# Performance work log

Hardware: AMD Instinct MI355X
Metric: run time of the kernel (lower is better)

The kernel has to match this reference:

```python
import jax, jax.numpy as jnp
import numpy as np

T, B = 4096, 32
EP_LEN = 256
K = T // EP_LEN          # episodes per trajectory
LM = EP_LEN              # max episode length
S_DIM, C_DIM, M_DIM, L_DIM = 128, 32, 32, 32
E_S, E_C, H, A = 128, 64, 256, 16


def setup_inputs() -> dict:
    key = jax.random.key(0)
    ks = jax.random.split(key, 16)
    f = lambda i, shape: jax.random.normal(ks[i], shape, jnp.float32)
    inp = {
        "state": f(0, (T, B, S_DIM)),
        "latent_mean": f(1, (T, B, L_DIM)) * 0.1,
        "latent_logvar": f(2, (T, B, L_DIM)) * 0.1,
        "latent_mean_t": f(3, (T, B, L_DIM)) * 0.1,
        "latent_logvar_t": f(4, (T, B, L_DIM)) * 0.1,
        "agent_character": f(5, (T, B, C_DIM)),
        "mental_state": f(6, (T, B, M_DIM)),
        "partner_actions": jax.random.randint(ks[7], (LM, B), 0, A, jnp.int32),
    }
    # episode boundaries: done at the last step of each EP_LEN-long episode
    t = jnp.arange(T)
    inp["dones"] = jnp.broadcast_to(((t + 1) % EP_LEN == 0).astype(jnp.float32)[:, None], (T, B))
    sc = lambda fan: 1.0 / np.sqrt(fan)
    inp["W_se"] = f(8, (S_DIM, E_S)) * sc(S_DIM); inp["b_se"] = jnp.zeros((E_S,), jnp.float32)
    inp["W_ce"] = f(9, (C_DIM, E_C)) * sc(C_DIM); inp["b_ce"] = jnp.zeros((E_C,), jnp.float32)
    inp["W_sa"] = f(10, (E_S + E_C, H)) * sc(E_S + E_C); inp["b_sa"] = jnp.zeros((H,), jnp.float32)
    inp["W_h"] = f(11, (E_C + M_DIM, H)) * sc(E_C + M_DIM); inp["b_h"] = jnp.zeros((H,), jnp.float32)
    inp["Wi"] = f(12, (H, 3 * H)) * sc(H); inp["bi"] = jnp.zeros((3 * H,), jnp.float32)
    inp["Wh"] = f(13, (H, 3 * H)) * sc(H); inp["bh"] = jnp.zeros((3 * H,), jnp.float32)
    inp["W_out"] = f(14, (H, A)) * sc(H); inp["b_out"] = jnp.zeros((A,), jnp.float32)
    return inp


def _gru(h, x, Wi, bi, Wh, bh):
    gi = x @ Wi + bi
    gh = h @ Wh + bh
    ir, iz, inn = jnp.split(gi, 3, axis=-1)
    hr, hz, hn = jnp.split(gh, 3, axis=-1)
    r = jax.nn.sigmoid(ir + hr)
    z = jax.nn.sigmoid(iz + hz)
    n = jnp.tanh(inn + r * hn)
    return (1.0 - z) * n + z * h


def _episode_layout(d):  # d: [T] float dones -> (episode_id, pos_in_episode)
    started = jnp.concatenate([jnp.zeros((1,), bool), d[:-1] > 0.5])
    ep = jnp.cumsum(started.astype(jnp.int32))
    t = jnp.arange(d.shape[0])
    start = jax.lax.cummax(jnp.where(started, t, 0))
    return ep, t - start


def _to_episodes(x, ep, pos):  # x: [T, F] -> [K, LM, F]  (transform_timestep_to_batch)
    return jnp.zeros((K, LM) + x.shape[1:], x.dtype).at[ep, pos].set(x, mode="drop")


def _shift_padding_to_front(out, mask):  # out: [K, LM, D], mask: [K, LM]
    cnt = mask.sum(-1).astype(jnp.int32)
    src = jnp.arange(LM)[None, :] - (LM - cnt)[:, None]
    idx = jnp.clip(src, 0, LM - 1)
    ok = (src >= 0).astype(out.dtype)
    shifted = jnp.take_along_axis(out, idx[:, :, None], axis=1) * ok[:, :, None]
    return shifted, jnp.take_along_axis(mask, idx, axis=1) * ok


def _forward(state, latent_mean, latent_logvar, latent_mean_t, latent_logvar_t,
             agent_character, mental_state, partner_actions, dones,
             W_se, b_se, W_ce, b_ce, W_sa, b_sa, W_h, b_h, Wi, bi, Wh, bh, W_out, b_out):
    # ---- KL between consecutive-timestep posteriors ----
    lm = jnp.concatenate((latent_mean, latent_mean_t), axis=-1)
    lv = jnp.concatenate((latent_logvar, latent_logvar_t), axis=-1)
    gauss_dim = lm.shape[-1]
    all_m = jnp.concatenate((jnp.zeros((1,) + lm.shape[1:], lm.dtype), lm), axis=0)
    all_lv = jnp.concatenate((jnp.zeros((1,) + lv.shape[1:], lv.dtype), lv), axis=0)
    mu, m = all_m[1:], all_m[:-1]
    logE, logS = all_lv[1:], all_lv[:-1]
    kl = 0.5 * (jnp.sum(logS, -1) - jnp.sum(logE, -1) - gauss_dim
                + jnp.sum(jnp.exp(logE - logS), -1)
                + jnp.sum((m - mu) * (m - mu) / jnp.exp(logS), -1))  # [T,B]
    kl_loss = kl.sum(0).sum(0).mean()

    # ---- embeddings ----
    se = jax.nn.relu(state @ W_se + b_se)                         # [T,B,E_S]
    ce = jax.nn.relu(agent_character @ W_ce + b_ce)               # [T,B,E_C]
    sa = jnp.concatenate((se, ce), -1) @ W_sa + b_sa              # [T,B,H]
    hid = jnp.concatenate((ce, mental_state), -1) @ W_h + b_h     # [T,B,H]

    # ---- split trajectories into episodes (gather/scatter) ----
    ep, pos = jax.vmap(_episode_layout, in_axes=1, out_axes=0)(dones)  # [B,T] each
    to_ep = jax.vmap(_to_episodes, in_axes=(1, 0, 0), out_axes=0)
    k_sa = to_ep(sa, ep, pos)                                     # [B,K,LM,H]
    k_hid = to_ep(hid, ep, pos)                                   # [B,K,LM,H]
    k_d = to_ep(dones[..., None], ep, pos)[..., 0]                # [B,K,LM]
    mask = jax.vmap(lambda e, p: jnp.zeros((K, LM), jnp.float32).at[e, p].set(1.0, mode="drop"))(ep, pos)

    # ---- sequential RNN scan per episode (vectorized over B*K) ----
    h0 = k_hid[:, :, 0, :]                                        # [B,K,H]
    xs = (jnp.moveaxis(k_sa, 2, 0), jnp.moveaxis(k_hid, 2, 0), jnp.moveaxis(k_d, 2, 0))

    def step(h, xt):
        sa_t, hid_t, d_t = xt
        h = jnp.where(d_t[..., None] > 0.5, hid_t, h)             # reset to per-step init on done
        h = _gru(h, sa_t, Wi, bi, Wh, bh)
        return h, h

    _, ys = jax.lax.scan(step, h0, xs)                            # [LM,B,K,H]
    ys = jnp.moveaxis(ys, 0, 2)                                   # [B,K,LM,H]

    logits = (ys @ W_out + b_out) * mask[..., None]               # [B,K,LM,A]
    shifted, _ = jax.vmap(_shift_padding_to_front)(logits, mask)
    out = jnp.moveaxis(shifted.sum(1), 0, 1)                      # [LM,B,A]

    logp = jnp.take_along_axis(jax.nn.log_softmax(out, -1), partner_actions[..., None], -1)[..., 0]
    return kl_loss, logp.sum(-1)                                  # scalar, [LM]


def reference(state, latent_mean, latent_logvar, latent_mean_t, latent_logvar_t,
              agent_character, mental_state, partner_actions, dones,
              W_se, b_se, W_ce, b_ce, W_sa, b_sa, W_h, b_h, Wi, bi, Wh, bh, W_out, b_out):
    return _forward(state, latent_mean, latent_logvar, latent_mean_t, latent_logvar_t,
                    agent_character, mental_state, partner_actions, dones,
                    W_se, b_se, W_ce, b_ce, W_sa, b_sa, W_h, b_h, Wi, bi, Wh, bh, W_out, b_out)
```

## Files before the change

### kernel.cpp

```cpp
#include <hip/hip_runtime.h>
#include <math.h>

typedef short bf16x8 __attribute__((ext_vector_type(8)));
typedef float f32x4 __attribute__((ext_vector_type(4)));
typedef unsigned short u16;
typedef unsigned int u32;

#define T_DIM 4096
#define B_DIM 32

static constexpr size_t OFF_SE     = 0;
static constexpr size_t OFF_CE     = 33554432;
static constexpr size_t OFF_SA     = 50331648;
static constexpr size_t OFF_HID    = 117440512;
static constexpr size_t OFF_WHT    = 117964800;
static constexpr size_t OFF_WIT    = 118358016;
static constexpr size_t OFF_OUTACC = 118751232;
static constexpr size_t OFF_KLP    = 119799808;

__device__ __forceinline__ u16 f2bf(float x) {
    u32 b = __float_as_uint(x);
    u32 lsb = (b >> 16) & 1u;
    b += 0x7fffu + lsb;
    return (u16)(b >> 16);
}
__device__ __forceinline__ float bf2f(u16 u) {
    return __uint_as_float(((u32)u) << 16);
}
__device__ __forceinline__ float fsig(float x) {
    x = fminf(fmaxf(x, -30.f), 30.f);
    float e = __expf(x);
    return __fdividef(e, e + 1.f);
}
__device__ __forceinline__ float ftanh(float x) {
    x = fminf(fmaxf(x, -15.f), 15.f);
    float e = __expf(2.f * x);
    return __fdividef(e - 1.f, e + 1.f);
}

__global__ __launch_bounds__(256) void prep_kernel(const float* __restrict__ Wh,
                                                   const float* __restrict__ Wi,
                                                   u16* __restrict__ WhT,
                                                   u16* __restrict__ WiT) {
    int idx = blockIdx.x * 256 + threadIdx.x;
    if (idx < 196608) {
        int n = idx >> 8, k = idx & 255;
        WhT[idx] = f2bf(Wh[k * 768 + n]);
    } else {
        int i = idx - 196608;
        int n = i >> 8, k = i & 255;
        WiT[i] = f2bf(Wi[k * 768 + n]);
    }
}

__global__ __launch_bounds__(256) void prep2_kernel(const float* __restrict__ Wse,
                                                    const float* __restrict__ Wce,
                                                    const float* __restrict__ Wsa,
                                                    const float* __restrict__ Wwh,
                                                    u16* __restrict__ WTse,
                                                    u16* __restrict__ WTce,
                                                    u16* __restrict__ WTsa,
                                                    u16* __restrict__ WTh) {
    int idx = blockIdx.x * 256 + threadIdx.x;
    if (idx < 16384) {
        int n = idx >> 7, k = idx & 127;
        WTse[n * 128 + k] = f2bf(Wse[k * 128 + n]);
    } else if (idx < 18432) {
        int i = idx - 16384;
        int n = i >> 5, k = i & 31;
        WTce[n * 32 + k] = f2bf(Wce[k * 64 + n]);
    } else if (idx < 67584) {
        int i = idx - 18432;
        int n = i / 192, k = i % 192;
        WTsa[n * 192 + k] = f2bf(Wsa[k * 256 + n]);
    } else {
        int i = idx - 67584;
        int n = i / 96, k = i % 96;
        WTh[n * 96 + k] = f2bf(Wwh[k * 256 + n]);
    }
}

#define KLTERM(MU, LE, M, LS)                   \
    do {                                        \
        float _ls = (LS), _le = (LE);           \
        sS += _ls; sE += _le;                   \
        float _es = expf(-_ls);                 \
        sX += expf(_le) * _es;                  \
        float _dm = (M) - (MU);                 \
        sQ += _dm * _dm * _es;                  \
    } while (0)

__global__ __launch_bounds__(256) void kl_kernel(const float* __restrict__ lm,
                                                 const float* __restrict__ lv,
                                                 const float* __restrict__ lmt,
                                                 const float* __restrict__ lvt,
                                                 float* __restrict__ klp) {
    __shared__ float red[256];
    int tid = threadIdx.x;
    int idx = blockIdx.x * 256 + tid;
    float sS = 0.f, sE = 0.f, sX = 0.f, sQ = 0.f;
    const int cur = idx * 32;
    const int prv = cur - B_DIM * 32;
    const bool hasprev = (idx >= B_DIM);
    for (int half = 0; half < 2; half++) {
        const float* pm = half ? lmt : lm;
        const float* pv = half ? lvt : lv;
        for (int ch = 0; ch < 8; ch++) {
            float4 mu = *(const float4*)&pm[cur + ch * 4];
            float4 le = *(const float4*)&pv[cur + ch * 4];
            float4 m = make_float4(0.f, 0.f, 0.f, 0.f);
            float4 ls = make_float4(0.f, 0.f, 0.f, 0.f);
            if (hasprev) {
                m = *(const float4*)&pm[prv + ch * 4];
                ls = *(const float4*)&pv[prv + ch * 4];
            }
            KLTERM(mu.x, le.x, m.x, ls.x);
            KLTERM(mu.y, le.y, m.y, ls.y);
            KLTERM(mu.z, le.z, m.z, ls.z);
            KLTERM(mu.w, le.w, m.w, ls.w);
        }
    }
    float kl = 0.5f * (sS - sE - 64.0f + sX + sQ);
    red[tid] = kl;
    __syncthreads();
    for (int s = 128; s > 0; s >>= 1) {
        if (tid < s) red[tid] += red[tid + s];
        __syncthreads();
    }
    if (tid == 0) klp[blockIdx.x] = red[0];
}

__global__ __launch_bounds__(256) void gemm_k(const float* __restrict__ A32a,
                                              const u16* __restrict__ A16a,
                                              const u16* __restrict__ A16b,
                                              const u16* __restrict__ WT,
                                              const float* __restrict__ bias,
                                              u16* __restrict__ out,
                                              int mode, int K, int N, int do_relu) {
    __shared__ __align__(16) u16 As[64 * 40];
    const int tid = threadIdx.x;
    const int rows0 = blockIdx.x * 64;
    const int cols0 = blockIdx.y * 64;
    const int w16 = tid >> 6;
    const int lane = tid & 63;
    const int quad = lane >> 4;
    const int l15 = lane & 15;
    f32x4 acc[4];
    for (int i = 0; i < 4; i++) acc[i] = (f32x4){0.f, 0.f, 0.f, 0.f};
    const int nsteps = K >> 5;
    const int arow = tid >> 2, aseg = (tid & 3) << 3;
    for (int ks = 0; ks < nsteps; ks++) {
        const int grow = rows0 + arow;
        const int k0 = ks * 32 + aseg;
        if (mode == 0) {
            float4 v0 = *(const float4*)&A32a[grow * 128 + k0];
            float4 v1 = *(const float4*)&A32a[grow * 128 + k0 + 4];
            u16* d = &As[arow * 40 + aseg];
            d[0] = f2bf(v0.x); d[1] = f2bf(v0.y); d[2] = f2bf(v0.z); d[3] = f2bf(v0.w);
            d[4] = f2bf(v1.x); d[5] = f2bf(v1.y); d[6] = f2bf(v1.z); d[7] = f2bf(v1.w);
        } else if (mode == 1) {
            float4 v0 = *(const float4*)&A32a[grow * 32 + k0];
            float4 v1 = *(const float4*)&A32a[grow * 32 + k0 + 4];
            u16* d = &As[arow * 40 + aseg];
            d[0] = f2bf(v0.x); d[1] = f2bf(v0.y); d[2] = f2bf(v0.z); d[3] = f2bf(v0.w);
            d[4] = f2bf(v1.x); d[5] = f2bf(v1.y); d[6] = f2bf(v1.z); d[7] = f2bf(v1.w);
        } else if (mode == 2) {
            bf16x8 v = (k0 < 128) ? *(const bf16x8*)&A16a[grow * 128 + k0]
                                  : *(const bf16x8*)&A16b[grow * 64 + (k0 - 128)];
            *(bf16x8*)&As[arow * 40 + aseg] = v;
        } else {
            const int k6 = grow >> 6, w = (grow >> 5) & 1, bb = grow & 31;
            const int trow = (k6 * 256 + w * 255) * B_DIM + bb;
            for (int j = 0; j < 8; j++) {
                const int k = k0 + j;
                float v = (k < 64) ? bf2f(A16a[trow * 64 + k]) : A32a[trow * 32 + (k - 64)];
                As[arow * 40 + aseg + j] = f2bf(v);
            }
        }
        __syncthreads();
        bf16x8 af = *(const bf16x8*)&As[(w16 * 16 + l15) * 40 + quad * 8];
        const int kb = ks * 32 + quad * 8;
#pragma unroll
        for (int nt = 0; nt < 4; nt++) {
            bf16x8 bfr = *(const bf16x8*)&WT[(size_t)(cols0 + nt * 16 + l15) * K + kb];
            acc[nt] = __builtin_amdgcn_mfma_f32_16x16x32_bf16(af, bfr, acc[nt], 0, 0, 0);
        }
        __syncthreads();
    }
    for (int nt = 0; nt < 4; nt++) {
        const int c = cols0 + nt * 16 + l15;
        const float bv = bias[c];
        for (int r = 0; r < 4; r++) {
            const int row = rows0 + w16 * 16 + quad * 4 + r;
            float v = acc[nt][r] + bv;
            if (do_relu) v = fmaxf(v, 0.f);
            out[row * N + c] = f2bf(v);
        }
    }
}

__global__ void __launch_bounds__(512)
__attribute__((amdgpu_waves_per_eu(2, 2)))
gru6_kernel(const u16* __restrict__ hid,
            const u16* __restrict__ sa,
            const u16* __restrict__ WhT,
            const u16* __restrict__ WiT,
            const float* __restrict__ Wout,
            const float* __restrict__ bi,
            const float* __restrict__ bh,
            u16* __restrict__ gic_all,
            float* __restrict__ outacc) {
    __shared__ __align__(16) u16 whL[8 * 16 * 264];
    __shared__ __align__(16) u16 stage[64 * 264];
    __shared__ __align__(16) u16 hB[16 * 264];
    __shared__ __align__(16) u16 WoL[16 * 264];
    __shared__ __align__(16) float logL[32 * 16];
    __shared__ float bfold[768];
    __shared__ float bhnL[256];
    const int blk = blockIdx.x;
    const int b = blk >> 1, half = blk & 1;
    const int tid = threadIdx.x;
    const int lane = tid & 63, wv = tid >> 6;
    const int quad = lane >> 4, l15 = lane & 15;
    const int c0 = (tid & 63) * 4;
    u16* gic = gic_all + (size_t)blk * (256 * 768);

    for (int i = tid; i < 4096; i += 512) {
        const int s = i >> 9, rr = (i >> 5) & 15, seg = (i & 31) * 8;
        const int g = s * 6 + 5;
        *(bf16x8*)&whL[(s * 16 + rr) * 264 + seg] = *(const bf16x8*)&WhT[(g * 16 + rr) * 256 + seg];
    }
    for (int i = tid; i < 4096; i += 512) {
        const int a = i >> 8, k = i & 255;
        WoL[a * 264 + k] = f2bf(Wout[k * 16 + a]);
    }
    for (int c = tid; c < 768; c += 512) bfold[c] = (c < 512) ? (bi[c] + bh[c]) : bi[c];
    if (tid < 256) bhnL[tid] = bh[512 + tid];
    float hreg[4];
    {
        ushort4 hv = *(const ushort4*)&hid[(size_t)((((half << 3) + wv) << 6) + b) * 256 + c0];
        hreg[0] = bf2f(hv.x); hreg[1] = bf2f(hv.y);
        hreg[2] = bf2f(hv.z); hreg[3] = bf2f(hv.w);
        *(ushort4*)&hB[wv * 264 + c0] = hv;
        ushort4 z = make_ushort4(0, 0, 0, 0);
        *(ushort4*)&hB[(8 + wv) * 264 + c0] = z;
    }
    __syncthreads();

    bf16x8 wreg[5][8];
    for (int ch = 0; ch < 8; ch++) {
        for (int as = 0; as < 4; as++) {
            __syncthreads();
#pragma unroll
            for (int j = 0; j < 4; j++) {
                const int lin = j * 512 + tid;
                const int row = lin >> 5, seg = (lin & 31) * 8;
                const int pcs = as * 8 + (row >> 3), sql = row & 7;
                const int t = ((half << 3) + sql) * 256 + ch * 32 + pcs;
                *(bf16x8*)&stage[row * 264 + seg] =
                    *(const bf16x8*)&sa[((size_t)(t * 32 + b)) * 256 + seg];
            }
            __syncthreads();
            bf16x8 afr[4][8];
#pragma unroll
            for (int mt = 0; mt < 4; mt++)
#pragma unroll
                for (int ks = 0; ks < 8; ks++)
                    afr[mt][ks] = *(const bf16x8*)&stage[(mt * 16 + l15) * 264 + ks * 32 + quad * 8];
            bf16x8 wc[8], wn[8];
            {
                const u16* p = &WiT[((wv * 6) * 16 + l15) * 256 + quad * 8];
#pragma unroll
                for (int ks = 0; ks < 8; ks++) wc[ks] = *(const bf16x8*)&p[ks * 32];
            }
            for (int j = 0; j < 6; j++) {
                if (j < 5) {
                    const u16* p = &WiT[((wv * 6 + j + 1) * 16 + l15) * 256 + quad * 8];
#pragma unroll
                    for (int ks = 0; ks < 8; ks++) wn[ks] = *(const bf16x8*)&p[ks * 32];
                }
                const float bf = bfold[(wv * 6 + j) * 16 + l15];
#pragma unroll
                for (int mt = 0; mt < 4; mt++) {
                    f32x4 acc = (f32x4){0.f, 0.f, 0.f, 0.f};
#pragma unroll
                    for (int ks = 0; ks < 8; ks++)
                        acc = __builtin_amdgcn_mfma_f32_16x16x32_bf16(afr[mt][ks], wc[ks], acc, 0, 0, 0);
                    const int rbase = as * 64 + mt * 16 + quad * 4;
#pragma unroll
                    for (int r = 0; r < 4; r++)
                        gic[(size_t)(rbase + r) * 768 + (wv * 6 + j) * 16 + l15] = f2bf(acc[r] + bf);
                }
#pragma unroll
                for (int ks = 0; ks < 8; ks++) wc[ks] = wn[ks];
            }
        }
#pragma unroll
        for (int j = 0; j < 5; j++) {
            const u16* p = &WhT[((wv * 6 + j) * 16 + l15) * 256 + quad * 8];
#pragma unroll
            for (int ks = 0; ks < 8; ks++) wreg[j][ks] = *(const bf16x8*)&p[ks * 32];
        }
        __syncthreads();
        ushort4 pregi0, pregi1, pregi2;
        {
            const u16* gp0 = &gic[(size_t)(0 * 8 + wv) * 768];
            pregi0 = *(const ushort4*)&gp0[c0];
            pregi1 = *(const ushort4*)&gp0[256 + c0];
            pregi2 = *(const ushort4*)&gp0[512 + c0];
        }
        for (int pc = 0; pc < 32; pc++) {
            const int POS = ch * 32 + pc;
            __syncthreads();
            ushort4 g_r = pregi0;
            ushort4 g_z = pregi1;
            ushort4 g_n = pregi2;
            if (pc < 31) {
                const u16* gp = &gic[(size_t)((pc + 1) * 8 + wv) * 768];
                pregi0 = *(const ushort4*)&gp[c0];
                pregi1 = *(const ushort4*)&gp[256 + c0];
                pregi2 = *(const ushort4*)&gp[512 + c0];
            }
            bf16x8 af[8];
            if (POS == 255) {
                const u16* hp = &hid[(size_t)((((half << 3) + (l15 & 7)) << 6) + 32 + b) * 256 + quad * 8];
#pragma unroll
                for (int ks = 0; ks < 8; ks++) af[ks] = *(const bf16x8*)&hp[ks * 32];
            } else {
#pragma unroll
                for (int ks = 0; ks < 8; ks++)
                    af[ks] = *(const bf16x8*)&hB[l15 * 264 + ks * 32 + quad * 8];
            }
            if (wv == 7) {
                f32x4 acc = (f32x4){0.f, 0.f, 0.f, 0.f};
                if (POS == 255) {
#pragma unroll
                    for (int ks = 0; ks < 8; ks++) {
                        bf16x8 al = *(const bf16x8*)&hB[l15 * 264 + ks * 32 + quad * 8];
                        bf16x8 wo = *(const bf16x8*)&WoL[l15 * 264 + ks * 32 + quad * 8];
                        acc = __builtin_amdgcn_mfma_f32_16x16x32_bf16(al, wo, acc, 0, 0, 0);
                    }
                } else {
#pragma unroll
                    for (int ks = 0; ks < 8; ks++) {
                        bf16x8 wo = *(const bf16x8*)&WoL[l15 * 264 + ks * 32 + quad * 8];
                        acc = __builtin_amdgcn_mfma_f32_16x16x32_bf16(af[ks], wo, acc, 0, 0, 0);
                    }
                }
                float s = acc[0] + acc[1] + acc[2] + acc[3];
                s += __shfl_down(s, 32);
                s += __shfl_down(s, 16);
                if (lane < 16)
                    logL[(((pc + 31) & 31) << 4) + lane] = s;
            }
#pragma unroll
            for (int j = 0; j < 5; j++) {
                f32x4 acc = (f32x4){0.f, 0.f, 0.f, 0.f};
#pragma unroll
                for (int ks = 0; ks < 8; ks++)
                    acc = __builtin_amdgcn_mfma_f32_16x16x32_bf16(af[ks], wreg[j][ks], acc, 0, 0, 0);
                const int t = wv * 6 + j;
#pragma unroll
                for (int r = 0; r < 4; r++)
                    stage[(quad * 4 + r) * 776 + t * 16 + l15] = f2bf(acc[r]);
            }
            {
                const u16* p = &whL[(wv * 16 + l15) * 264 + quad * 8];
                f32x4 acc = (f32x4){0.f, 0.f, 0.f, 0.f};
#pragma unroll
                for (int ks = 0; ks < 8; ks++)
                    acc = __builtin_amdgcn_mfma_f32_16x16x32_bf16(af[ks], *(const bf16x8*)&p[ks * 32], acc, 0, 0, 0);
                const int t = wv * 6 + 5;
#pragma unroll
                for (int r = 0; r < 4; r++)
                    stage[(quad * 4 + r) * 776 + t * 16 + l15] = f2bf(acc[r]);
            }
            __syncthreads();
            if (POS == 255) {
                ushort4 hv = *(const ushort4*)&hid[(size_t)((((half << 3) + wv) << 6) + 32 + b) * 256 + c0];
                hreg[0] = bf2f(hv.x); hreg[1] = bf2f(hv.y);
                hreg[2] = bf2f(hv.z); hreg[3] = bf2f(hv.w);
            }
            ushort4 h_r = *(const ushort4*)&stage[wv * 776 + c0];
            ushort4 h_z = *(const ushort4*)&stage[wv * 776 + 256 + c0];
            ushort4 h_n = *(const ushort4*)&stage[wv * 776 + 512 + c0];
            const u16* grp = (const u16*)&g_r; const u16* gzp = (const u16*)&g_z;
            const u16* gnp = (const u16*)&g_n;
            const u16* hrp = (const u16*)&h_r; const u16* hzp = (const u16*)&h_z;
            const u16* hnp = (const u16*)&h_n;
            ushort4 hp4;
            u16* ho = (u16*)&hp4;
#pragma unroll
            for (int j = 0; j < 4; j++) {
                const float rv = fsig(bf2f(grp[j]) + bf2f(hrp[j]));
                const float zv = fsig(bf2f(gzp[j]) + bf2f(hzp[j]));
                const float nv = ftanh(bf2f(gnp[j]) + rv * (bf2f(hnp[j]) + bhnL[c0 + j]));
                hreg[j] = (1.f - zv) * nv + zv * hreg[j];
                ho[j] = f2bf(hreg[j]);
            }
            *(ushort4*)&hB[wv * 264 + c0] = hp4;
        }
        if (wv == 7) {
            const int s = lane >> 1, aoff = (lane & 1) << 3;
            const int P = (s == 31) ? (ch * 32 - 1) : (ch * 32 + s);
            if (P >= 0) {
                const float4* lp = (const float4*)&logL[(s << 4) + aoff];
                float* gpo = outacc + (size_t)half * 131072 + ((size_t)P * B_DIM + b) * 16 + aoff;
                *(float4*)&gpo[0] = lp[0];
                *(float4*)&gpo[4] = lp[1];
            }
        }
    }
    __syncthreads();
    if (wv == 7) {
        f32x4 acc = (f32x4){0.f, 0.f, 0.f, 0.f};
#pragma unroll
        for (int ks = 0; ks < 8; ks++) {
            bf16x8 al = *(const bf16x8*)&hB[l15 * 264 + ks * 32 + quad * 8];
            bf16x8 wo = *(const bf16x8*)&WoL[l15 * 264 + ks * 32 + quad * 8];
            acc = __builtin_amdgcn_mfma_f32_16x16x32_bf16(al, wo, acc, 0, 0, 0);
        }
        float s = acc[0] + acc[1] + acc[2] + acc[3];
        s += __shfl_down(s, 32);
        s += __shfl_down(s, 16);
        if (lane < 16)
            outacc[(size_t)half * 131072 + ((size_t)255 * B_DIM + b) * 16 + lane] = s;
    }
}

__global__ __launch_bounds__(64) void final_kernel(const float* __restrict__ outacc,
                                                   const int* __restrict__ pa,
                                                   const float* __restrict__ klp,
                                                   const float* __restrict__ bout,
                                                   float* __restrict__ dout) {
    const int lane = threadIdx.x;
    if (blockIdx.x == 256) {
        float s = 0.f;
        for (int j = 0; j < 8; j++) s += klp[lane + 64 * j];
        for (int off = 32; off > 0; off >>= 1) s += __shfl_down(s, off);
        if (lane == 0) dout[0] = s;
        return;
    }
    const int pos = blockIdx.x;
    float lp = 0.f;
    if (lane < 32) {
        const float* r0 = outacc + ((size_t)pos * B_DIM + lane) * 16;
        const float* r1 = r0 + 131072;
        float v[16];
        float mx = -1e30f;
#pragma unroll
        for (int a = 0; a < 16; a++) {
            v[a] = r0[a] + r1[a] + 16.0f * bout[a];
            mx = fmaxf(mx, v[a]);
        }
        float s = 0.f;
#pragma unroll
        for (int a = 0; a < 16; a++) s += expf(v[a] - mx);
        const int ai = pa[pos * B_DIM + lane];
        lp = v[ai] - mx - logf(s);
    }
    for (int off = 16; off > 0; off >>= 1) lp += __shfl_down(lp, off);
    if (lane == 0) dout[1 + pos] = lp;
}

extern "C" void kernel_launch(void* const* d_in, const int* in_sizes, int n_in,
                              void* d_out, int out_size, void* d_ws, size_t ws_size,
                              hipStream_t stream) {
    const float* state = (const float*)d_in[0];
    const float* lm    = (const float*)d_in[1];
    const float* lv    = (const float*)d_in[2];
    const float* lmt   = (const float*)d_in[3];
    const float* lvt   = (const float*)d_in[4];
    const float* ach   = (const float*)d_in[5];
    const float* ms    = (const float*)d_in[6];
    const int*   pa    = (const int*)d_in[7];
    const float* W_se  = (const float*)d_in[9];
    const float* b_se  = (const float*)d_in[10];
    const float* W_ce  = (const float*)d_in[11];
    const float* b_ce  = (const float*)d_in[12];
    const float* W_sa  = (const float*)d_in[13];
    const float* b_sa  = (const float*)d_in[14];
    const float* W_h   = (const float*)d_in[15];
    const float* b_h   = (const float*)d_in[16];
    const float* Wi    = (const float*)d_in[17];
    const float* bi    = (const float*)d_in[18];
    const float* Wh    = (const float*)d_in[19];
    const float* bh    = (const float*)d_in[20];
    const float* Wout  = (const float*)d_in[21];
    const float* bout  = (const float*)d_in[22];

    char* ws = (char*)d_ws;
    u16* se   = (u16*)(ws + OFF_SE);
    u16* ce   = (u16*)(ws + OFF_CE);
    u16* sa   = (u16*)(ws + OFF_SA);
    u16* hid  = (u16*)(ws + OFF_HID);
    u16* WhT  = (u16*)(ws + OFF_WHT);
    u16* WiT  = (u16*)(ws + OFF_WIT);
    u16* WT_se = (u16*)(ws + OFF_OUTACC);
    u16* WT_ce = (u16*)(ws + OFF_OUTACC + 32768);
    u16* WT_sa = (u16*)(ws + OFF_OUTACC + 36864);
    u16* WT_h  = (u16*)(ws + OFF_OUTACC + 135168);
    float* outacc = (float*)(ws + OFF_OUTACC);
    float* klp    = (float*)(ws + OFF_KLP);
    float* dout   = (float*)d_out;

    prep_kernel<<<1536, 256, 0, stream>>>(Wh, Wi, WhT, WiT);
    prep2_kernel<<<360, 256, 0, stream>>>(W_se, W_ce, W_sa, W_h, WT_se, WT_ce, WT_sa, WT_h);
    kl_kernel<<<512, 256, 0, stream>>>(lm, lv, lmt, lvt, klp);
    gemm_k<<<dim3(2048, 2), 256, 0, stream>>>(state, nullptr, nullptr, WT_se, b_se, se, 0, 128, 128, 1);
    gemm_k<<<dim3(2048, 1), 256, 0, stream>>>(ach, nullptr, nullptr, WT_ce, b_ce, ce, 1, 32, 64, 1);
    gemm_k<<<dim3(2048, 4), 256, 0, stream>>>(nullptr, se, ce, WT_sa, b_sa, sa, 2, 192, 256, 0);
    gemm_k<<<dim3(16, 4), 256, 0, stream>>>(ms, ce, nullptr, WT_h, b_h, hid, 5, 96, 256, 0);
    gru6_kernel<<<64, 512, 0, stream>>>(hid, sa, WhT, WiT, Wout, bi, bh, se, outacc);
    final_kernel<<<257, 64, 0, stream>>>(outacc, pa, klp, bout, dout);
}
```

Measured before the change: 1.762 ms.

## Stage GEMM weights in LDS, drop gic prefetch and logit buffering in GRU

The GEMM kernel now stages each weight tile into shared memory with one coalesced load per thread, where before every wave read weight fragments straight from global memory. In the GRU kernel, the software prefetch of the next step's input-gate values is removed, so those loads are issued in the same step that uses them. Logits are also written directly to global memory each step instead of being buffered in LDS and flushed once per chunk. The changes trade register pressure and an extra barrier against load latency and scattered small global stores inside the serial recurrence.

```diff
diff --git a/kernel.cpp b/kernel.cpp
--- a/kernel.cpp
+++ b/kernel.cpp
@@ -138,6 +138,7 @@
                                               u16* __restrict__ out,
                                               int mode, int K, int N, int do_relu) {
     __shared__ __align__(16) u16 As[64 * 40];
+    __shared__ __align__(16) u16 Bs[64 * 40];
     const int tid = threadIdx.x;
     const int rows0 = blockIdx.x * 64;
     const int cols0 = blockIdx.y * 64;
@@ -149,6 +150,7 @@
     for (int i = 0; i < 4; i++) acc[i] = (f32x4){0.f, 0.f, 0.f, 0.f};
     const int nsteps = K >> 5;
     const int arow = tid >> 2, aseg = (tid & 3) << 3;
+    const int brow = tid >> 2, bseg = (tid & 3) << 3;
     for (int ks = 0; ks < nsteps; ks++) {
         const int grow = rows0 + arow;
         const int k0 = ks * 32 + aseg;
@@ -177,12 +179,14 @@
                 As[arow * 40 + aseg + j] = f2bf(v);
             }
         }
+        {
+            bf16x8 wv8 = *(const bf16x8*)&WT[(size_t)(cols0 + brow) * K + ks * 32 + bseg];
+            *(bf16x8*)&Bs[brow * 40 + bseg] = wv8;
+        }
         __syncthreads();
         bf16x8 af = *(const bf16x8*)&As[(w16 * 16 + l15) * 40 + quad * 8];
-        const int kb = ks * 32 + quad * 8;
-#pragma unroll
         for (int nt = 0; nt < 4; nt++) {
-            bf16x8 bfr = *(const bf16x8*)&WT[(size_t)(cols0 + nt * 16 + l15) * K + kb];
+            bf16x8 bfr = *(const bf16x8*)&Bs[(nt * 16 + l15) * 40 + quad * 8];
             acc[nt] = __builtin_amdgcn_mfma_f32_16x16x32_bf16(af, bfr, acc[nt], 0, 0, 0);
         }
         __syncthreads();
@@ -214,7 +218,6 @@
     __shared__ __align__(16) u16 stage[64 * 264];
     __shared__ __align__(16) u16 hB[16 * 264];
     __shared__ __align__(16) u16 WoL[16 * 264];
-    __shared__ __align__(16) float logL[32 * 16];
     __shared__ float bfold[768];
     __shared__ float bhnL[256];
     const int blk = blockIdx.x;
@@ -301,26 +304,13 @@
 #pragma unroll
             for (int ks = 0; ks < 8; ks++) wreg[j][ks] = *(const bf16x8*)&p[ks * 32];
         }
-        __syncthreads();
-        ushort4 pregi0, pregi1, pregi2;
-        {
-            const u16* gp0 = &gic[(size_t)(0 * 8 + wv) * 768];
-            pregi0 = *(const ushort4*)&gp0[c0];
-            pregi1 = *(const ushort4*)&gp0[256 + c0];
-            pregi2 = *(const ushort4*)&gp0[512 + c0];
-        }
         for (int pc = 0; pc < 32; pc++) {
             const int POS = ch * 32 + pc;
             __syncthreads();
-            ushort4 g_r = pregi0;
-            ushort4 g_z = pregi1;
-            ushort4 g_n = pregi2;
-            if (pc < 31) {
-                const u16* gp = &gic[(size_t)((pc + 1) * 8 + wv) * 768];
-                pregi0 = *(const ushort4*)&gp[c0];
-                pregi1 = *(const ushort4*)&gp[256 + c0];
-                pregi2 = *(const ushort4*)&gp[512 + c0];
-            }
+            const u16* gp = &gic[(size_t)(pc * 8 + wv) * 768];
+            ushort4 g_r = *(const ushort4*)&gp[c0];
+            ushort4 g_z = *(const ushort4*)&gp[256 + c0];
+            ushort4 g_n = *(const ushort4*)&gp[512 + c0];
             bf16x8 af[8];
             if (POS == 255) {
                 const u16* hp = &hid[(size_t)((((half << 3) + (l15 & 7)) << 6) + 32 + b) * 256 + quad * 8];
@@ -331,27 +321,19 @@
                 for (int ks = 0; ks < 8; ks++)
                     af[ks] = *(const bf16x8*)&hB[l15 * 264 + ks * 32 + quad * 8];
             }
-            if (wv == 7) {
+            if (wv == 7 && POS > 0) {
                 f32x4 acc = (f32x4){0.f, 0.f, 0.f, 0.f};
-                if (POS == 255) {
-#pragma unroll
-                    for (int ks = 0; ks < 8; ks++) {
-                        bf16x8 al = *(const bf16x8*)&hB[l15 * 264 + ks * 32 + quad * 8];
-                        bf16x8 wo = *(const bf16x8*)&WoL[l15 * 264 + ks * 32 + quad * 8];
-                        acc = __builtin_amdgcn_mfma_f32_16x16x32_bf16(al, wo, acc, 0, 0, 0);
-                    }
-                } else {
-#pragma unroll
-                    for (int ks = 0; ks < 8; ks++) {
-                        bf16x8 wo = *(const bf16x8*)&WoL[l15 * 264 + ks * 32 + quad * 8];
-                        acc = __builtin_amdgcn_mfma_f32_16x16x32_bf16(af[ks], wo, acc, 0, 0, 0);
-                    }
+#pragma unroll
+                for (int ks = 0; ks < 8; ks++) {
+                    bf16x8 al = *(const bf16x8*)&hB[l15 * 264 + ks * 32 + quad * 8];
+                    bf16x8 wo = *(const bf16x8*)&WoL[l15 * 264 + ks * 32 + quad * 8];
+                    acc = __builtin_amdgcn_mfma_f32_16x16x32_bf16(al, wo, acc, 0, 0, 0);
                 }
                 float s = acc[0] + acc[1] + acc[2] + acc[3];
                 s += __shfl_down(s, 32);
                 s += __shfl_down(s, 16);
                 if (lane < 16)
-                    logL[(((pc + 31) & 31) << 4) + lane] = s;
+                    outacc[(size_t)half * 131072 + ((size_t)(POS - 1) * B_DIM + b) * 16 + lane] = s;
             }
 #pragma unroll
             for (int j = 0; j < 5; j++) {
@@ -399,16 +381,6 @@
                 ho[j] = f2bf(hreg[j]);
             }
             *(ushort4*)&hB[wv * 264 + c0] = hp4;
-        }
-        if (wv == 7) {
-            const int s = lane >> 1, aoff = (lane & 1) << 3;
-            const int P = (s == 31) ? (ch * 32 - 1) : (ch * 32 + s);
-            if (P >= 0) {
-                const float4* lp = (const float4*)&logL[(s << 4) + aoff];
-                float* gpo = outacc + (size_t)half * 131072 + ((size_t)P * B_DIM + b) * 16 + aoff;
-                *(float4*)&gpo[0] = lp[0];
-                *(float4*)&gpo[4] = lp[1];
-            }
         }
     }
     __syncthreads();
```

Measured after the change: 1.645 ms. -6.6%, faster.
